# Optimization experiments

Hardware: AMD Instinct MI355X
Metric: run time of the kernel (lower is better)

The kernel has to match this reference:

```python
import jax, jax.numpy as jnp
import numpy as np

B, D, H, W, C = 4, 8, 56, 56, 128
NH = 4
WS = (2, 7, 7)   # window size (d, h, w)
SS = (1, 3, 3)   # shift size
HD = C // NH
MLP_HIDDEN = 4 * C


def _window_partition(x, ws):
    # x: (b, d, h, w, c) -> (b*nW, wd*wh*ww, c)
    b, d, h, w, c = x.shape
    wd, wh, ww = ws
    x = x.reshape(b, d // wd, wd, h // wh, wh, w // ww, ww, c)
    return x.transpose(0, 1, 3, 5, 2, 4, 6, 7).reshape(-1, wd * wh * ww, c)


def _window_reverse(win, ws, b, d, h, w):
    wd, wh, ww = ws
    x = win.reshape(b, d // wd, h // wh, w // ww, wd, wh, ww, -1)
    return x.transpose(0, 1, 4, 2, 5, 3, 6, 7).reshape(b, d, h, w, -1)


def _layernorm(x, g, b, eps=1e-5):
    mu = jnp.mean(x, axis=-1, keepdims=True)
    var = jnp.var(x, axis=-1, keepdims=True)
    return (x - mu) * jax.lax.rsqrt(var + eps) * g + b


def setup_inputs() -> dict:
    key = jax.random.key(0)
    ks = jax.random.split(key, 10)
    wd, wh, ww = WS
    sd, sh, sw = SS
    N = wd * wh * ww

    x = jax.random.normal(ks[0], (B, D, H, W, C), jnp.float32)

    # ---- attention mask for cyclic shift (compute_mask) ----
    img = np.zeros((1, D, H, W, 1), np.float32)
    cnt = 0
    for dsl in (slice(0, -wd), slice(-wd, -sd), slice(-sd, None)):
        for hsl in (slice(0, -wh), slice(-wh, -sh), slice(-sh, None)):
            for wsl in (slice(0, -ww), slice(-ww, -sw), slice(-sw, None)):
                img[:, dsl, hsl, wsl, :] = cnt
                cnt += 1
    mw = img.reshape(1, D // wd, wd, H // wh, wh, W // ww, ww, 1)
    mw = mw.transpose(0, 1, 3, 5, 2, 4, 6, 7).reshape(-1, N)  # (nW, N)
    am = mw[:, None, :] - mw[:, :, None]
    mask = jnp.asarray(np.where(am != 0, -100.0, 0.0).astype(np.float32))

    # ---- relative position index (buffer) ----
    coords = np.stack(np.meshgrid(np.arange(wd), np.arange(wh), np.arange(ww),
                                  indexing='ij')).reshape(3, -1)
    rel = (coords[:, :, None] - coords[:, None, :]).transpose(1, 2, 0)
    rel[..., 0] += wd - 1
    rel[..., 1] += wh - 1
    rel[..., 2] += ww - 1
    rel[..., 0] *= (2 * wh - 1) * (2 * ww - 1)
    rel[..., 1] *= (2 * ww - 1)
    rel_index = jnp.asarray(rel.sum(-1).astype(np.int32))  # (N, N)

    s = 0.02
    n_bias = (2 * wd - 1) * (2 * wh - 1) * (2 * ww - 1)
    return {
        'x': x,
        'mask': mask,
        'rel_index': rel_index,
        'norm1_g': jnp.ones((C,), jnp.float32),
        'norm1_b': jnp.zeros((C,), jnp.float32),
        'qkv_w': s * jax.random.normal(ks[1], (3 * C, C), jnp.float32),
        'qkv_b': jnp.zeros((3 * C,), jnp.float32),
        'rpb': s * jax.random.normal(ks[2], (n_bias, NH), jnp.float32),
        'proj_w': s * jax.random.normal(ks[3], (C, C), jnp.float32),
        'proj_b': jnp.zeros((C,), jnp.float32),
        'norm2_g': jnp.ones((C,), jnp.float32),
        'norm2_b': jnp.zeros((C,), jnp.float32),
        'fc1_w': s * jax.random.normal(ks[4], (MLP_HIDDEN, C), jnp.float32),
        'fc1_b': jnp.zeros((MLP_HIDDEN,), jnp.float32),
        'fc2_w': s * jax.random.normal(ks[5], (C, MLP_HIDDEN), jnp.float32),
        'fc2_b': jnp.zeros((C,), jnp.float32),
    }


def reference(x, mask, rel_index, norm1_g, norm1_b, qkv_w, qkv_b, rpb,
              proj_w, proj_b, norm2_g, norm2_b, fc1_w, fc1_b, fc2_w, fc2_b):
    shortcut = x
    # ---- part1: norm -> shift -> window attention -> reverse ----
    y = _layernorm(x, norm1_g, norm1_b)
    # dims divisible by window: no padding. Cyclic shift.
    y = jnp.roll(y, (-SS[0], -SS[1], -SS[2]), axis=(1, 2, 3))
    xw = _window_partition(y, WS)                      # (Bn, N, C)
    Bn, N, _ = xw.shape
    qkv = xw @ qkv_w.T + qkv_b                         # (Bn, N, 3C)
    qkv = qkv.reshape(Bn, N, 3, NH, HD).transpose(2, 0, 3, 1, 4)
    q = qkv[0] * (HD ** -0.5)
    k, v = qkv[1], qkv[2]
    attn = jnp.einsum('bhnd,bhmd->bhnm', q, k)         # (Bn, NH, N, N)
    bias = rpb[rel_index.reshape(-1)].reshape(N, N, NH).transpose(2, 0, 1)
    attn = attn + bias[None]
    nW = mask.shape[0]
    attn = attn.reshape(Bn // nW, nW, NH, N, N) + mask[None, :, None]
    attn = jax.nn.softmax(attn, axis=-1).reshape(Bn, NH, N, N)
    out = jnp.einsum('bhnm,bhmd->bhnd', attn, v)
    out = out.transpose(0, 2, 1, 3).reshape(Bn, N, C)
    out = out @ proj_w.T + proj_b
    y = _window_reverse(out, WS, B, D, H, W)
    y = jnp.roll(y, SS, axis=(1, 2, 3))
    x = shortcut + y
    # ---- part2: MLP ----
    h1 = _layernorm(x, norm2_g, norm2_b)
    h1 = jax.nn.gelu(h1 @ fc1_w.T + fc1_b, approximate=False)
    x = x + (h1 @ fc2_w.T + fc2_b)
    return x
```

## Files before the change

### kernel.cpp

```cpp
#include <hip/hip_runtime.h>
#include <hip/hip_bf16.h>
#include <math.h>

using bf16 = __hip_bfloat16;
typedef __attribute__((ext_vector_type(8))) short short8;
typedef __attribute__((ext_vector_type(4))) float float4v;
typedef __attribute__((ext_vector_type(4))) unsigned short ushort4v;

#define DEVI __device__ __forceinline__

constexpr int Nc = 98;
constexpr int NWIN = 256;
constexpr int BNc = 4 * NWIN;
constexpr int NTOK = 4 * 8 * 56 * 56;

DEVI float b2f(bf16 v) { return __bfloat162float(v); }
DEVI short f2bs(float v) { bf16 h = __float2bfloat16(v); return *reinterpret_cast<short*>(&h); }

DEVI float4v mfma16(short8 a, short8 b, float4v c) {
    return __builtin_amdgcn_mfma_f32_16x16x32_bf16(a, b, c, 0, 0, 0);
}

DEVI void gload16(const short* g, short* lds_base) {
    __builtin_amdgcn_global_load_lds((const __attribute__((address_space(1))) unsigned int*)g,
                                     (__attribute__((address_space(3))) unsigned int*)lds_base,
                                     16, 0, 0);
}

__global__ __launch_bounds__(256) void k_wconv(const float* __restrict__ qw, const float* __restrict__ pw,
                                               const float* __restrict__ f1, const float* __restrict__ f2,
                                               short* __restrict__ wbf) {
    int i = blockIdx.x * 256 + threadIdx.x;
    float v;
    if (i < 49152) v = qw[i];
    else if (i < 65536) v = pw[i - 49152];
    else if (i < 131072) v = f1[i - 65536];
    else v = f2[i - 131072];
    wbf[i] = f2bs(v);
}

__global__ __launch_bounds__(256) void k_cmb(const int* __restrict__ relidx, const float* __restrict__ rpb,
                                             const float* __restrict__ mask, short* __restrict__ cmbT) {
    int elem = blockIdx.x * 256 + threadIdx.x;
    int sl = blockIdx.y;
    int wc = sl >> 2, head = sl & 3;
    int j = elem / 112, i = elem - j * 112;
    float v;
    if (j >= 98)      v = -1e30f;
    else if (i >= 98) v = 0.f;
    else              v = rpb[relidx[i * 98 + j] * 4 + head] + mask[(size_t)wc * 9604 + i * 98 + j];
    cmbT[(size_t)sl * 12544 + elem] = f2bs(v);
}

__global__ __launch_bounds__(256) void k_ln1_win(const float* __restrict__ x,
                                                 const float* __restrict__ g,
                                                 const float* __restrict__ bta,
                                                 bf16* __restrict__ xw) {
    int wave = (blockIdx.x * 256 + threadIdx.x) >> 6;
    int lane = threadIdx.x & 63;
    int win = wave / Nc, n = wave % Nc;
    int bb = win >> 8;
    int rem = win & 255;
    int dblk = rem >> 6, hblk = (rem >> 3) & 7, wblk = rem & 7;
    int wd = n / 49, r49 = n % 49, wh = r49 / 7, ww = r49 % 7;
    int d = dblk * 2 + wd, h = hblk * 7 + wh, w = wblk * 7 + ww;
    int ds = d + 1;  if (ds >= 8)  ds -= 8;
    int hs = h + 3;  if (hs >= 56) hs -= 56;
    int wsp = w + 3; if (wsp >= 56) wsp -= 56;
    size_t src = ((((size_t)bb * 8 + ds) * 56 + hs) * 56 + wsp) * 128;
    int c = lane * 2;
    float2 v = *reinterpret_cast<const float2*>(x + src + c);
    float v0 = v.x, v1 = v.y;
    float s = v0 + v1, sq = v0 * v0 + v1 * v1;
    #pragma unroll
    for (int off = 32; off; off >>= 1) { s += __shfl_xor(s, off); sq += __shfl_xor(sq, off); }
    float mean = s * (1.0f / 128.0f);
    float var  = sq * (1.0f / 128.0f) - mean * mean;
    float inv  = rsqrtf(var + 1e-5f);
    size_t dst = (size_t)wave * 128 + c;
    xw[dst]     = __float2bfloat16((v0 - mean) * inv * g[c]     + bta[c]);
    xw[dst + 1] = __float2bfloat16((v1 - mean) * inv * g[c + 1] + bta[c + 1]);
}

template<int K, int EPI, typename OutT>
__global__ __launch_bounds__(256) void k_gemm_mfma(const short* __restrict__ A,
                                                   const short* __restrict__ Bw,
                                                   const float* __restrict__ bias,
                                                   const float* __restrict__ res,
                                                   OutT* __restrict__ out, int Ncols) {
    __shared__ __align__(16) short smem[128 * 136];
    short* sA = smem;
    short* sB = smem + 8192;
    int t = threadIdx.x;
    int lane = t & 63, wid = t >> 6;
    int wm = wid >> 1, wn = wid & 1;
    int rsub = lane >> 3;
    int csl  = lane & 7;
    int m0 = blockIdx.x * 128, n0 = blockIdx.y * 128;
    float4v acc[4][4];
    #pragma unroll
    for (int a = 0; a < 4; ++a)
        #pragma unroll
        for (int b = 0; b < 4; ++b) acc[a][b] = (float4v){0.f, 0.f, 0.f, 0.f};

    for (int k0 = 0; k0 < K; k0 += 64) {
        #pragma unroll
        for (int v = 0; v < 4; ++v) {
            int row = (wid * 4 + v) * 8 + rsub;
            int ch = csl ^ (row & 7);
            gload16(A + (size_t)(m0 + row) * K + k0 + ch * 8, sA + (wid * 4 + v) * 512);
            gload16(Bw + (size_t)(n0 + row) * K + k0 + ch * 8, sB + (wid * 4 + v) * 512);
        }
        __syncthreads();
        #pragma unroll
        for (int kk = 0; kk < 2; ++kk) {
            int crb = kk * 4 + (lane >> 4);
            short8 af[4], bfr[4];
            #pragma unroll
            for (int mf = 0; mf < 4; ++mf) {
                int row = wm * 64 + mf * 16 + (lane & 15);
                af[mf] = *reinterpret_cast<const short8*>(&sA[row * 64 + (crb ^ (row & 7)) * 8]);
            }
            #pragma unroll
            for (int nf = 0; nf < 4; ++nf) {
                int row = wn * 64 + nf * 16 + (lane & 15);
                bfr[nf] = *reinterpret_cast<const short8*>(&sB[row * 64 + (crb ^ (row & 7)) * 8]);
            }
            #pragma unroll
            for (int mf = 0; mf < 4; ++mf)
                #pragma unroll
                for (int nf = 0; nf < 4; ++nf)
                    acc[mf][nf] = mfma16(af[mf], bfr[nf], acc[mf][nf]);
        }
        __syncthreads();
    }
    if constexpr (sizeof(OutT) == 2) {
        #pragma unroll
        for (int nf = 0; nf < 4; ++nf) {
            int col = wn * 64 + nf * 16 + (lane & 15);
            int gcol = n0 + col;
            float bv = bias[gcol];
            #pragma unroll
            for (int mf = 0; mf < 4; ++mf) {
                #pragma unroll
                for (int r = 0; r < 4; ++r) {
                    int row = wm * 64 + mf * 16 + (lane >> 4) * 4 + r;
                    float v = acc[mf][nf][r] + bv;
                    if (EPI == 0) { if (gcol < 128) v *= 0.17677669529663689f; }
                    else if (EPI == 2) { v = 0.5f * v * (1.0f + erff(v * 0.7071067811865475f)); }
                    smem[row * 136 + col] = f2bs(v);
                }
            }
        }
        __syncthreads();
        #pragma unroll
        for (int p = 0; p < 8; ++p) {
            int row = p * 16 + (t >> 4);
            int c0 = (t & 15) * 8;
            uint4 val = *reinterpret_cast<const uint4*>(&smem[row * 136 + c0]);
            *reinterpret_cast<uint4*>(out + (size_t)(m0 + row) * Ncols + n0 + c0) = val;
        }
    } else {
        #pragma unroll
        for (int mf = 0; mf < 4; ++mf) {
            #pragma unroll
            for (int nf = 0; nf < 4; ++nf) {
                int col = n0 + wn * 64 + nf * 16 + (lane & 15);
                float bv = bias[col];
                #pragma unroll
                for (int r = 0; r < 4; ++r) {
                    size_t row = m0 + wm * 64 + mf * 16 + (lane >> 4) * 4 + r;
                    float v = acc[mf][nf][r] + bv;
                    if (EPI == 3) v += res[row * 128 + col];
                    out[row * Ncols + col] = v;
                }
            }
        }
    }
}

__global__ __launch_bounds__(256, 4) void k_attn_mfma(const bf16* __restrict__ qkv,
                                                      const short* __restrict__ cmbT,
                                                      bf16* __restrict__ aout) {
    constexpr int QP = 40;
    constexpr int VP = 136;
    constexpr int PP = 136;
    __shared__ __align__(16) char smem[8704 + 30464];
    short* sVT = (short*)smem;
    short* sQ  = (short*)(smem + 8704);
    short* sK  = (short*)(smem + 8704 + 8960);
    short* sP  = (short*)(smem + 8704);
    int t = threadIdx.x, lane = t & 63, wid = t >> 6;
    int win = blockIdx.x >> 2, head = blockIdx.x & 3;
    const bf16* base = qkv + (size_t)win * Nc * 384 + head * 32;

    for (int idx = t; idx < Nc * 4; idx += 256) {
        int i = idx >> 2, g = idx & 3;
        uint4 q4 = *reinterpret_cast<const uint4*>(base + (size_t)i * 384 + g * 8);
        uint4 k4 = *reinterpret_cast<const uint4*>(base + (size_t)i * 384 + 128 + g * 8);
        uint4 v4 = *reinterpret_cast<const uint4*>(base + (size_t)i * 384 + 256 + g * 8);
        *reinterpret_cast<uint4*>(&sQ[i * QP + g * 8]) = q4;
        *reinterpret_cast<uint4*>(&sK[i * QP + g * 8]) = k4;
        const short* vp = reinterpret_cast<const short*>(&v4);
        #pragma unroll
        for (int e = 0; e < 8; ++e) sVT[(g * 8 + e) * VP + i] = vp[e];
    }
    for (int idx = t; idx < 14 * QP; idx += 256) {
        int r = 98 + idx / QP, c = idx % QP;
        sQ[r * QP + c] = 0; sK[r * QP + c] = 0;
    }
    for (int idx = t; idx < 32 * 30; idx += 256) {
        int d = idx / 30, c = 98 + idx % 30;
        sVT[d * VP + c] = 0;
    }
    __syncthreads();

    float4v s[2][7];
    #pragma unroll
    for (int mi = 0; mi < 2; ++mi)
        #pragma unroll
        for (int fn = 0; fn < 7; ++fn) s[mi][fn] = (float4v){0.f, 0.f, 0.f, 0.f};
    short8 qf[2];
    #pragma unroll
    for (int mi = 0; mi < 2; ++mi) {
        if (wid * 2 + mi < 7) {
            int row = (wid * 2 + mi) * 16 + (lane & 15);
            qf[mi] = *reinterpret_cast<const short8*>(&sQ[row * QP + (lane >> 4) * 8]);
        }
    }
    #pragma unroll
    for (int fn = 0; fn < 7; ++fn) {
        short8 kf = *reinterpret_cast<const short8*>(&sK[(fn * 16 + (lane & 15)) * QP + (lane >> 4) * 8]);
        #pragma unroll
        for (int mi = 0; mi < 2; ++mi) {
            if (wid * 2 + mi < 7) s[mi][fn] = mfma16(qf[mi], kf, s[mi][fn]);
        }
    }

    const unsigned short* cb = (const unsigned short*)(cmbT + (size_t)((win & 255) * 4 + head) * 12544);
    #pragma unroll
    for (int mi = 0; mi < 2; ++mi) {
        if (wid * 2 + mi >= 7) continue;
        int i0 = (wid * 2 + mi) * 16 + (lane >> 4) * 4;
        #pragma unroll
        for (int fn = 0; fn < 7; ++fn) {
            int j = fn * 16 + (lane & 15);
            ushort4v bm4 = *reinterpret_cast<const ushort4v*>(cb + j * 112 + i0);
            #pragma unroll
            for (int r = 0; r < 4; ++r) {
                union { unsigned u; float f; } cv; cv.u = ((unsigned)bm4[r]) << 16;
                s[mi][fn][r] = __expf(s[mi][fn][r] + cv.f);
            }
        }
        #pragma unroll
        for (int r = 0; r < 4; ++r) {
            float sum = 0.f;
            #pragma unroll
            for (int fn = 0; fn < 7; ++fn) sum += s[mi][fn][r];
            #pragma unroll
            for (int m = 1; m <= 8; m <<= 1) sum += __shfl_xor(sum, m);
            float inv = 1.0f / sum;
            #pragma unroll
            for (int fn = 0; fn < 7; ++fn) s[mi][fn][r] *= inv;
        }
    }
    __syncthreads();

    for (int idx = t; idx < 112 * 16; idx += 256) {
        int rr = idx >> 4, c2 = 112 + (idx & 15);
        sP[rr * PP + c2] = 0;
    }
    #pragma unroll
    for (int mi = 0; mi < 2; ++mi) {
        if (wid * 2 + mi >= 7) continue;
        int i0 = (wid * 2 + mi) * 16 + (lane >> 4) * 4;
        #pragma unroll
        for (int r = 0; r < 4; ++r) {
            #pragma unroll
            for (int fn = 0; fn < 7; ++fn) {
                int j = fn * 16 + (lane & 15);
                sP[(i0 + r) * PP + j] = f2bs(s[mi][fn][r]);
            }
        }
    }
    __syncthreads();

    float4v o[2][2];
    #pragma unroll
    for (int mi = 0; mi < 2; ++mi)
        #pragma unroll
        for (int nd = 0; nd < 2; ++nd) o[mi][nd] = (float4v){0.f, 0.f, 0.f, 0.f};
    #pragma unroll
    for (int jc = 0; jc < 4; ++jc) {
        short8 pf[2];
        #pragma unroll
        for (int mi = 0; mi < 2; ++mi) {
            if (wid * 2 + mi < 7) {
                int row = (wid * 2 + mi) * 16 + (lane & 15);
                pf[mi] = *reinterpret_cast<const short8*>(&sP[row * PP + jc * 32 + (lane >> 4) * 8]);
            }
        }
        #pragma unroll
        for (int nd = 0; nd < 2; ++nd) {
            short8 vf = *reinterpret_cast<const short8*>(&sVT[(nd * 16 + (lane & 15)) * VP + jc * 32 + (lane >> 4) * 8]);
            #pragma unroll
            for (int mi = 0; mi < 2; ++mi) {
                if (wid * 2 + mi < 7) o[mi][nd] = mfma16(pf[mi], vf, o[mi][nd]);
            }
        }
    }
    bf16* obase = aout + (size_t)win * Nc * 128 + head * 32;
    #pragma unroll
    for (int mi = 0; mi < 2; ++mi) {
        if (wid * 2 + mi >= 7) continue;
        #pragma unroll
        for (int nd = 0; nd < 2; ++nd) {
            int d = nd * 16 + (lane & 15);
            #pragma unroll
            for (int r = 0; r < 4; ++r) {
                int i = (wid * 2 + mi) * 16 + (lane >> 4) * 4 + r;
                if (i < 98) obase[(size_t)i * 128 + d] = __float2bfloat16(o[mi][nd][r]);
            }
        }
    }
}

__global__ __launch_bounds__(256) void k_resid_ln2(const float* __restrict__ x,
                                                   const bf16* __restrict__ pt,
                                                   const float* __restrict__ g,
                                                   const float* __restrict__ bta,
                                                   float* __restrict__ x1,
                                                   bf16* __restrict__ xn2) {
    int tok = (blockIdx.x * 256 + threadIdx.x) >> 6;
    int lane = threadIdx.x & 63;
    int ww = tok % 56; int t2 = tok / 56;
    int hh = t2 % 56;  int t3 = t2 / 56;
    int dd = t3 & 7;   int bb = t3 >> 3;
    int d = dd + 7;  if (d >= 8)  d -= 8;
    int h = hh + 53; if (h >= 56) h -= 56;
    int w = ww + 53; if (w >= 56) w -= 56;
    int win = ((bb * 4 + (d >> 1)) * 8 + h / 7) * 8 + w / 7;
    int n = (d & 1) * 49 + (h % 7) * 7 + (w % 7);
    int c = lane * 2;
    const bf16* pp = pt + ((size_t)win * Nc + n) * 128 + c;
    float2 xv = *reinterpret_cast<const float2*>(x + (size_t)tok * 128 + c);
    float v0 = xv.x + b2f(pp[0]);
    float v1 = xv.y + b2f(pp[1]);
    *reinterpret_cast<float2*>(x1 + (size_t)tok * 128 + c) = float2{v0, v1};
    float s = v0 + v1, sq = v0 * v0 + v1 * v1;
    #pragma unroll
    for (int off = 32; off; off >>= 1) { s += __shfl_xor(s, off); sq += __shfl_xor(sq, off); }
    float mean = s * (1.0f / 128.0f);
    float var  = sq * (1.0f / 128.0f) - mean * mean;
    float inv  = rsqrtf(var + 1e-5f);
    xn2[(size_t)tok * 128 + c]     = __float2bfloat16((v0 - mean) * inv * g[c]     + bta[c]);
    xn2[(size_t)tok * 128 + c + 1] = __float2bfloat16((v1 - mean) * inv * g[c + 1] + bta[c + 1]);
}

extern "C" void kernel_launch(void* const* d_in, const int* in_sizes, int n_in,
                              void* d_out, int out_size, void* d_ws, size_t ws_size,
                              hipStream_t stream) {
    const float* x      = (const float*)d_in[0];
    const float* mask   = (const float*)d_in[1];
    const int*   relidx = (const int*)  d_in[2];
    const float* n1g    = (const float*)d_in[3];
    const float* n1b    = (const float*)d_in[4];
    const float* qkv_w  = (const float*)d_in[5];
    const float* qkv_b  = (const float*)d_in[6];
    const float* rpb    = (const float*)d_in[7];
    const float* proj_w = (const float*)d_in[8];
    const float* proj_b = (const float*)d_in[9];
    const float* n2g    = (const float*)d_in[10];
    const float* n2b    = (const float*)d_in[11];
    const float* fc1_w  = (const float*)d_in[12];
    const float* fc1_b  = (const float*)d_in[13];
    const float* fc2_w  = (const float*)d_in[14];
    const float* fc2_b  = (const float*)d_in[15];

    char* ws = (char*)d_ws;
    const size_t MB = 1024 * 1024;
    bf16*  xw   = (bf16*)(ws);
    bf16*  qkv  = (bf16*)(ws + 25 * MB);
    bf16*  aout = (bf16*)(ws + 99 * MB);
    bf16*  ptmp = (bf16*)(ws + 124 * MB);
    short* cmbT = (short*)(ws + 149 * MB);
    float* x1   = (float*)(ws);
    bf16*  xn2  = (bf16*)(ws + 50 * MB);
    bf16*  h1   = (bf16*)(ws + 75 * MB);
    short* wbf  = (short*)(ws + 174 * MB);
    float* out  = (float*)d_out;

    const short* wq = wbf;
    const short* wp = wbf + 49152;
    const short* w1 = wbf + 65536;
    const short* w2 = wbf + 131072;

    k_wconv<<<768, 256, 0, stream>>>(qkv_w, proj_w, fc1_w, fc2_w, wbf);
    k_cmb<<<dim3(49, 1024), 256, 0, stream>>>(relidx, rpb, mask, cmbT);
    k_ln1_win<<<NTOK / 4, 256, 0, stream>>>(x, n1g, n1b, xw);
    k_gemm_mfma<128, 0, bf16><<<dim3(NTOK / 128, 3), 256, 0, stream>>>((const short*)xw, wq, qkv_b, nullptr, qkv, 384);
    k_attn_mfma<<<BNc * 4, 256, 0, stream>>>(qkv, cmbT, aout);
    k_gemm_mfma<128, 1, bf16><<<dim3(NTOK / 128, 1), 256, 0, stream>>>((const short*)aout, wp, proj_b, nullptr, ptmp, 128);
    k_resid_ln2<<<NTOK / 4, 256, 0, stream>>>(x, ptmp, n2g, n2b, x1, xn2);
    k_gemm_mfma<128, 2, bf16><<<dim3(NTOK / 128, 4), 256, 0, stream>>>((const short*)xn2, w1, fc1_b, nullptr, h1, 512);
    k_gemm_mfma<512, 3, float><<<dim3(NTOK / 128, 1), 256, 0, stream>>>((const short*)h1, w2, fc2_b, x1, out, 128);
}
```

Measured before the change: 280.1 us.

## Fuse projection GEMM with residual and LayerNorm2, use tanh GELU

Replaces the projection GEMM and the separate residual+LayerNorm2 kernel with one kernel. It computes the projection, adds bias and the shortcut, reverses the window shift via a per-row token map, and computes the LayerNorm statistics across waves in shared memory. This removes the intermediate bf16 projection buffer round trip and one launch. The fc1 epilogue also switches from erf GELU to a tanh-based approximation to cut transcendental cost, which slightly changes numerics.

```diff
diff --git a/kernel.cpp b/kernel.cpp
--- a/kernel.cpp
+++ b/kernel.cpp
@@ -19,6 +19,15 @@
 
 DEVI float4v mfma16(short8 a, short8 b, float4v c) {
     return __builtin_amdgcn_mfma_f32_16x16x32_bf16(a, b, c, 0, 0, 0);
+}
+
+DEVI float gelu_tanh(float x) {
+    float t = 0.7978845608028654f * (x + 0.044715f * x * x * x);
+    float at = fabsf(t);
+    float e2 = __expf(-2.0f * at);
+    float th = (1.0f - e2) / (1.0f + e2);
+    th = copysignf(th, t);
+    return 0.5f * x * (1.0f + th);
 }
 
 DEVI void gload16(const short* g, short* lds_base) {
@@ -147,7 +156,7 @@
                     int row = wm * 64 + mf * 16 + (lane >> 4) * 4 + r;
                     float v = acc[mf][nf][r] + bv;
                     if (EPI == 0) { if (gcol < 128) v *= 0.17677669529663689f; }
-                    else if (EPI == 2) { v = 0.5f * v * (1.0f + erff(v * 0.7071067811865475f)); }
+                    else if (EPI == 2) { v = gelu_tanh(v); }
                     smem[row * 136 + col] = f2bs(v);
                 }
             }
@@ -174,6 +183,119 @@
                     if (EPI == 3) v += res[row * 128 + col];
                     out[row * Ncols + col] = v;
                 }
+            }
+        }
+    }
+}
+
+__global__ __launch_bounds__(256) void k_proj_fused(const short* __restrict__ A,
+                                                    const short* __restrict__ Bw,
+                                                    const float* __restrict__ bias,
+                                                    const float* __restrict__ x,
+                                                    const float* __restrict__ g,
+                                                    const float* __restrict__ bta,
+                                                    float* __restrict__ x1,
+                                                    bf16* __restrict__ xn2) {
+    __shared__ __align__(16) short smem[128 * 136];
+    short* sA = smem;
+    short* sB = smem + 8192;
+    int t = threadIdx.x;
+    int lane = t & 63, wid = t >> 6;
+    int wm = wid >> 1, wn = wid & 1;
+    int rsub = lane >> 3, csl = lane & 7;
+    int m0 = blockIdx.x * 128;
+    float4v acc[4][4];
+    #pragma unroll
+    for (int a = 0; a < 4; ++a)
+        #pragma unroll
+        for (int b = 0; b < 4; ++b) acc[a][b] = (float4v){0.f, 0.f, 0.f, 0.f};
+
+    for (int k0 = 0; k0 < 128; k0 += 64) {
+        #pragma unroll
+        for (int v = 0; v < 4; ++v) {
+            int row = (wid * 4 + v) * 8 + rsub;
+            int ch = csl ^ (row & 7);
+            gload16(A + (size_t)(m0 + row) * 128 + k0 + ch * 8, sA + (wid * 4 + v) * 512);
+            gload16(Bw + (size_t)row * 128 + k0 + ch * 8, sB + (wid * 4 + v) * 512);
+        }
+        __syncthreads();
+        #pragma unroll
+        for (int kk = 0; kk < 2; ++kk) {
+            int crb = kk * 4 + (lane >> 4);
+            short8 af[4], bfr[4];
+            #pragma unroll
+            for (int mf = 0; mf < 4; ++mf) {
+                int row = wm * 64 + mf * 16 + (lane & 15);
+                af[mf] = *reinterpret_cast<const short8*>(&sA[row * 64 + (crb ^ (row & 7)) * 8]);
+            }
+            #pragma unroll
+            for (int nf = 0; nf < 4; ++nf) {
+                int row = wn * 64 + nf * 16 + (lane & 15);
+                bfr[nf] = *reinterpret_cast<const short8*>(&sB[row * 64 + (crb ^ (row & 7)) * 8]);
+            }
+            #pragma unroll
+            for (int mf = 0; mf < 4; ++mf)
+                #pragma unroll
+                for (int nf = 0; nf < 4; ++nf)
+                    acc[mf][nf] = mfma16(af[mf], bfr[nf], acc[mf][nf]);
+        }
+        __syncthreads();
+    }
+
+    int*   tokmap = (int*)smem;
+    float* psum   = (float*)(smem + 256);
+    float* psq    = (float*)(smem + 768);
+    if (t < 128) {
+        int wr = m0 + t;
+        int win = wr / 98, n = wr - win * 98;
+        int bb = win >> 8, rem = win & 255;
+        int dblk = rem >> 6, hblk = (rem >> 3) & 7, wblk = rem & 7;
+        int wd = n / 49, r49 = n - wd * 49, wh = r49 / 7, ww = r49 - wh * 7;
+        int d = dblk * 2 + wd, h = hblk * 7 + wh, w = wblk * 7 + ww;
+        int dd = d + 1;  if (dd >= 8)  dd -= 8;
+        int hh = h + 3;  if (hh >= 56) hh -= 56;
+        int w2 = w + 3;  if (w2 >= 56) w2 -= 56;
+        tokmap[t] = ((bb * 8 + dd) * 56 + hh) * 56 + w2;
+    }
+    __syncthreads();
+
+    #pragma unroll
+    for (int mf = 0; mf < 4; ++mf) {
+        #pragma unroll
+        for (int r = 0; r < 4; ++r) {
+            int row = wm * 64 + mf * 16 + (lane >> 4) * 4 + r;
+            int tok = tokmap[row];
+            float s = 0.f, sq = 0.f;
+            #pragma unroll
+            for (int nf = 0; nf < 4; ++nf) {
+                int col = wn * 64 + nf * 16 + (lane & 15);
+                float vv = acc[mf][nf][r] + bias[col] + x[(size_t)tok * 128 + col];
+                acc[mf][nf][r] = vv;
+                s += vv; sq += vv * vv;
+            }
+            #pragma unroll
+            for (int m = 1; m <= 8; m <<= 1) { s += __shfl_xor(s, m); sq += __shfl_xor(sq, m); }
+            if ((lane & 15) == 0) { psum[row * 2 + wn] = s; psq[row * 2 + wn] = sq; }
+        }
+    }
+    __syncthreads();
+    #pragma unroll
+    for (int mf = 0; mf < 4; ++mf) {
+        #pragma unroll
+        for (int r = 0; r < 4; ++r) {
+            int row = wm * 64 + mf * 16 + (lane >> 4) * 4 + r;
+            int tok = tokmap[row];
+            float s  = psum[row * 2] + psum[row * 2 + 1];
+            float sq = psq[row * 2]  + psq[row * 2 + 1];
+            float mean = s * (1.0f / 128.0f);
+            float var  = sq * (1.0f / 128.0f) - mean * mean;
+            float inv  = rsqrtf(var + 1e-5f);
+            #pragma unroll
+            for (int nf = 0; nf < 4; ++nf) {
+                int col = wn * 64 + nf * 16 + (lane & 15);
+                float vv = acc[mf][nf][r];
+                x1[(size_t)tok * 128 + col] = vv;
+                xn2[(size_t)tok * 128 + col] = __float2bfloat16((vv - mean) * inv * g[col] + bta[col]);
             }
         }
     }
@@ -323,38 +445,6 @@
             }
         }
     }
-}
-
-__global__ __launch_bounds__(256) void k_resid_ln2(const float* __restrict__ x,
-                                                   const bf16* __restrict__ pt,
-                                                   const float* __restrict__ g,
-                                                   const float* __restrict__ bta,
-                                                   float* __restrict__ x1,
-                                                   bf16* __restrict__ xn2) {
-    int tok = (blockIdx.x * 256 + threadIdx.x) >> 6;
-    int lane = threadIdx.x & 63;
-    int ww = tok % 56; int t2 = tok / 56;
-    int hh = t2 % 56;  int t3 = t2 / 56;
-    int dd = t3 & 7;   int bb = t3 >> 3;
-    int d = dd + 7;  if (d >= 8)  d -= 8;
-    int h = hh + 53; if (h >= 56) h -= 56;
-    int w = ww + 53; if (w >= 56) w -= 56;
-    int win = ((bb * 4 + (d >> 1)) * 8 + h / 7) * 8 + w / 7;
-    int n = (d & 1) * 49 + (h % 7) * 7 + (w % 7);
-    int c = lane * 2;
-    const bf16* pp = pt + ((size_t)win * Nc + n) * 128 + c;
-    float2 xv = *reinterpret_cast<const float2*>(x + (size_t)tok * 128 + c);
-    float v0 = xv.x + b2f(pp[0]);
-    float v1 = xv.y + b2f(pp[1]);
-    *reinterpret_cast<float2*>(x1 + (size_t)tok * 128 + c) = float2{v0, v1};
-    float s = v0 + v1, sq = v0 * v0 + v1 * v1;
-    #pragma unroll
-    for (int off = 32; off; off >>= 1) { s += __shfl_xor(s, off); sq += __shfl_xor(sq, off); }
-    float mean = s * (1.0f / 128.0f);
-    float var  = sq * (1.0f / 128.0f) - mean * mean;
-    float inv  = rsqrtf(var + 1e-5f);
-    xn2[(size_t)tok * 128 + c]     = __float2bfloat16((v0 - mean) * inv * g[c]     + bta[c]);
-    xn2[(size_t)tok * 128 + c + 1] = __float2bfloat16((v1 - mean) * inv * g[c + 1] + bta[c + 1]);
 }
 
 extern "C" void kernel_launch(void* const* d_in, const int* in_sizes, int n_in,
@@ -382,7 +472,6 @@
     bf16*  xw   = (bf16*)(ws);
     bf16*  qkv  = (bf16*)(ws + 25 * MB);
     bf16*  aout = (bf16*)(ws + 99 * MB);
-    bf16*  ptmp = (bf16*)(ws + 124 * MB);
     short* cmbT = (short*)(ws + 149 * MB);
     float* x1   = (float*)(ws);
     bf16*  xn2  = (bf16*)(ws + 50 * MB);
@@ -400,8 +489,7 @@
     k_ln1_win<<<NTOK / 4, 256, 0, stream>>>(x, n1g, n1b, xw);
     k_gemm_mfma<128, 0, bf16><<<dim3(NTOK / 128, 3), 256, 0, stream>>>((const short*)xw, wq, qkv_b, nullptr, qkv, 384);
     k_attn_mfma<<<BNc * 4, 256, 0, stream>>>(qkv, cmbT, aout);
-    k_gemm_mfma<128, 1, bf16><<<dim3(NTOK / 128, 1), 256, 0, stream>>>((const short*)aout, wp, proj_b, nullptr, ptmp, 128);
-    k_resid_ln2<<<NTOK / 4, 256, 0, stream>>>(x, ptmp, n2g, n2b, x1, xn2);
+    k_proj_fused<<<NTOK / 128, 256, 0, stream>>>((const short*)aout, wp, proj_b, x, n2g, n2b, x1, xn2);
     k_gemm_mfma<128, 2, bf16><<<dim3(NTOK / 128, 4), 256, 0, stream>>>((const short*)xn2, w1, fc1_b, nullptr, h1, 512);
     k_gemm_mfma<512, 3, float><<<dim3(NTOK / 128, 1), 256, 0, stream>>>((const short*)h1, w2, fc2_b, x1, out, 128);
 }
```

New measurement: 282.5 us. No clear change (+0.9%).
